# Kernel tuning notes

Hardware: AMD Instinct MI355X
Metric: run time of the kernel (lower is better)

## Reference

```python
import jax, jax.numpy as jnp
import numpy as np

MARGIN = 0.3
NUM_CLASSES = 1000


def setup_inputs() -> dict:
    key = jax.random.key(0)
    k1, k2 = jax.random.split(key)
    B, D = 8192, 256
    inputs = jax.random.normal(k1, (B, D), dtype=jnp.float32)
    targets = jax.random.randint(k2, (B,), 0, NUM_CLASSES, dtype=jnp.int64)
    return {"inputs": inputs, "targets": targets}


def reference(inputs, targets):
    # Squared Euclidean pairwise distances: ||x_i||^2 + ||x_j||^2 - 2 x_i.x_j
    sq = jnp.sum(inputs * inputs, axis=1)                      # [B]
    dist = sq[:, None] + sq[None, :] - 2.0 * (inputs @ inputs.T)  # [B, B]

    # Hard mining: per-row max over positives (same label, incl. self),
    # min over negatives, exactly as the torch per-row masked max/min loop.
    pos_mask = targets[:, None] == targets[None, :]            # [B, B] bool
    neg_inf = jnp.float32(-jnp.inf)
    pos_inf = jnp.float32(jnp.inf)
    dist_ap = jnp.max(jnp.where(pos_mask, dist, neg_inf), axis=1)  # [B]
    dist_an = jnp.min(jnp.where(pos_mask, pos_inf, dist), axis=1)  # [B]

    # MarginRankingLoss(margin)(dist_an, dist_ap, y=1) = mean relu(ap - an + m)
    loss = jnp.mean(jax.nn.relu(dist_ap - dist_an + MARGIN))
    prec = jnp.mean((dist_an > dist_ap).astype(jnp.float32))
    return (loss, prec)
```

## Files before the change

### kernel.cpp

```cpp
#include <hip/hip_runtime.h>
#include <hip/hip_bf16.h>

#define B_N 8192
#define D_K 256
#define MARGIN 0.3f

typedef float f32x4 __attribute__((ext_vector_type(4)));
typedef short s16x8 __attribute__((ext_vector_type(8)));

__device__ __forceinline__ unsigned fkey(float f) {
    unsigned u = __float_as_uint(f);
    return (u & 0x80000000u) ? ~u : (u | 0x80000000u);
}
__device__ __forceinline__ float kval(unsigned k) {
    return (k & 0x80000000u) ? __uint_as_float(k ^ 0x80000000u)
                             : __uint_as_float(~k);
}

__device__ __forceinline__ void load_lds16(const unsigned short* g,
                                           unsigned short* l) {
    __builtin_amdgcn_global_load_lds(
        (const __attribute__((address_space(1))) unsigned int*)g,
        (__attribute__((address_space(3))) unsigned int*)l, 16, 0, 0);
}

__global__ __launch_bounds__(256) void prep_kernel(const float* __restrict__ X,
        float* __restrict__ sq, unsigned* __restrict__ apk,
        unsigned* __restrict__ ank, unsigned short* __restrict__ Xp,
        float* __restrict__ acc2) {
    int row  = (blockIdx.x << 2) + (threadIdx.x >> 6);
    int lane = threadIdx.x & 63;
    const float4 v = reinterpret_cast<const float4*>(X + (size_t)row * D_K)[lane];

    float xs[4] = {v.x, v.y, v.z, v.w};
    ushort4 hv;
    unsigned short* hp = &hv.x;
    float s = 0.f;
    #pragma unroll
    for (int i = 0; i < 4; ++i) {
        __hip_bfloat16 h = __float2bfloat16(xs[i]);
        hp[i] = *reinterpret_cast<unsigned short*>(&h);
        float hf = __bfloat162float(h);
        s = fmaf(hf, hf, s);
    }
    *reinterpret_cast<ushort4*>(Xp + (size_t)row * D_K + lane * 4) = hv;

    #pragma unroll
    for (int o = 32; o > 0; o >>= 1) s += __shfl_down(s, o, 64);
    if (lane == 0) {
        sq[row]  = s;
        apk[row] = 0u;
        ank[row] = 0xFFFFFFFFu;
    }
    if (blockIdx.x == 0 && threadIdx.x == 0) {
        acc2[0] = 0.f; acc2[1] = 0.f;
        reinterpret_cast<unsigned*>(acc2)[2] = 0u;
    }
}

#define BM 128
#define BN 128

__global__ __launch_bounds__(256, 4) void dist_kernel(
        const unsigned short* __restrict__ Xp,
        const int* __restrict__ tgt, const float* __restrict__ sq,
        unsigned* __restrict__ apk, unsigned* __restrict__ ank) {
    __shared__ unsigned short Atile[128 * 64];
    __shared__ unsigned short Btile[128 * 64];

    const int t    = threadIdx.x;
    const int lane = t & 63;
    const int wave = t >> 6;
    const int wrow = (wave >> 1) * 64;
    const int wcol = (wave & 1) * 64;
    const int fr   = lane & 15;
    const int quad = lane >> 4;
    const float INF = __int_as_float(0x7f800000);

    int tt = blockIdx.x;
    int bx = (int)((sqrtf(8.f * (float)tt + 1.f) - 1.f) * 0.5f);
    while ((bx + 1) * (bx + 2) / 2 <= tt) ++bx;
    while (bx * (bx + 1) / 2 > tt) --bx;
    int by = tt - bx * (bx + 1) / 2;
    const int bm = by * BM;
    const int bn = bx * BN;

    const unsigned short* ag[4];
    const unsigned short* bg[4];
    unsigned short* al[4];
    unsigned short* bl[4];
    #pragma unroll
    for (int j = 0; j < 4; ++j) {
        int g = wave * 64 + j * 256 + lane;
        int r = g >> 3, s0 = g & 7;
        int u = s0 ^ (r & 7);
        ag[j] = Xp + (size_t)(bm + r) * D_K + u * 8;
        bg[j] = Xp + (size_t)(bn + r) * D_K + u * 8;
        al[j] = Atile + g * 8;
        bl[j] = Btile + g * 8;
    }

    f32x4 acc[4][4];
    #pragma unroll
    for (int i = 0; i < 4; ++i)
        #pragma unroll
        for (int j = 0; j < 4; ++j) acc[i][j] = (f32x4){0.f, 0.f, 0.f, 0.f};

    #pragma unroll 1
    for (int win = 0; win < 4; ++win) {
        __syncthreads();
        const int wo = win * 64;
        #pragma unroll
        for (int j = 0; j < 4; ++j) {
            load_lds16(ag[j] + wo, al[j]);
            load_lds16(bg[j] + wo, bl[j]);
        }
        __syncthreads();

        s16x8 a[4][2], b[4][2];
        #pragma unroll
        for (int mi = 0; mi < 4; ++mi) {
            int rb = (wrow + mi * 16 + fr) * 64;
            #pragma unroll
            for (int h = 0; h < 2; ++h) {
                int s = (h * 4 + quad) ^ (fr & 7);
                a[mi][h] = *reinterpret_cast<const s16x8*>(&Atile[rb + s * 8]);
            }
        }
        #pragma unroll
        for (int ni = 0; ni < 4; ++ni) {
            int rb = (wcol + ni * 16 + fr) * 64;
            #pragma unroll
            for (int h = 0; h < 2; ++h) {
                int s = (h * 4 + quad) ^ (fr & 7);
                b[ni][h] = *reinterpret_cast<const s16x8*>(&Btile[rb + s * 8]);
            }
        }
        #pragma unroll
        for (int mi = 0; mi < 4; ++mi)
            #pragma unroll
            for (int ni = 0; ni < 4; ++ni) {
                acc[mi][ni] = __builtin_amdgcn_mfma_f32_16x16x32_bf16(
                    a[mi][0], b[ni][0], acc[mi][ni], 0, 0, 0);
                acc[mi][ni] = __builtin_amdgcn_mfma_f32_16x16x32_bf16(
                    a[mi][1], b[ni][1], acc[mi][ni], 0, 0, 0);
            }
    }

    int   ct[4]; float csq[4];
    #pragma unroll
    for (int ni = 0; ni < 4; ++ni) {
        int c = bn + wcol + ni * 16 + fr;
        ct[ni] = tgt[c]; csq[ni] = sq[c];
    }
    float cap[4], can[4];
    #pragma unroll
    for (int ni = 0; ni < 4; ++ni) { cap[ni] = -INF; can[ni] = INF; }

    #pragma unroll
    for (int mi = 0; mi < 4; ++mi) {
        #pragma unroll
        for (int reg = 0; reg < 4; ++reg) {
            int rl = wrow + mi * 16 + quad * 4 + reg;
            int rt = tgt[bm + rl]; float rsq = sq[bm + rl];
            float rap = -INF, ran = INF;
            #pragma unroll
            for (int ni = 0; ni < 4; ++ni) {
                float d = rsq + csq[ni] - 2.f * acc[mi][ni][reg];
                bool pos = (rt == ct[ni]);
                if (pos) { rap = fmaxf(rap, d); cap[ni] = fmaxf(cap[ni], d); }
                else     { ran = fminf(ran, d); can[ni] = fminf(can[ni], d); }
            }
            #pragma unroll
            for (int o = 1; o < 16; o <<= 1) {
                rap = fmaxf(rap, __shfl_xor(rap, o, 64));
                ran = fminf(ran, __shfl_xor(ran, o, 64));
            }
            if (fr == 0) {
                atomicMax(&apk[bm + rl], fkey(rap));
                atomicMin(&ank[bm + rl], fkey(ran));
            }
        }
    }
    #pragma unroll
    for (int ni = 0; ni < 4; ++ni) {
        #pragma unroll
        for (int o = 16; o < 64; o <<= 1) {
            cap[ni] = fmaxf(cap[ni], __shfl_xor(cap[ni], o, 64));
            can[ni] = fminf(can[ni], __shfl_xor(can[ni], o, 64));
        }
    }
    if (lane < 16) {
        #pragma unroll
        for (int ni = 0; ni < 4; ++ni) {
            int c = bn + wcol + ni * 16 + lane;
            atomicMax(&apk[c], fkey(cap[ni]));
            atomicMin(&ank[c], fkey(can[ni]));
        }
    }
}

__global__ __launch_bounds__(256) void final_kernel(const unsigned* __restrict__ apk,
        const unsigned* __restrict__ ank, float* __restrict__ acc2,
        float* __restrict__ out) {
    __shared__ float s_sum[4], s_cnt[4];
    int i = blockIdx.x * 256 + threadIdx.x;
    float ap = kval(apk[i]);
    float an = kval(ank[i]);
    float v  = ap - an + MARGIN;
    float sum = v > 0.f ? v : 0.f;
    float cnt = an > ap ? 1.f : 0.f;
    #pragma unroll
    for (int o = 32; o > 0; o >>= 1) {
        sum += __shfl_down(sum, o, 64);
        cnt += __shfl_down(cnt, o, 64);
    }
    int wave = threadIdx.x >> 6, lane = threadIdx.x & 63;
    if (lane == 0) { s_sum[wave] = sum; s_cnt[wave] = cnt; }
    __syncthreads();
    if (threadIdx.x == 0) {
        float ts = 0.f, tc = 0.f;
        #pragma unroll
        for (int w = 0; w < 4; ++w) { ts += s_sum[w]; tc += s_cnt[w]; }
        atomicAdd(&acc2[0], ts);
        atomicAdd(&acc2[1], tc);
        __threadfence();
        unsigned ticket = atomicAdd(reinterpret_cast<unsigned*>(acc2) + 2, 1u);
        if (ticket == gridDim.x - 1) {
            float fs = atomicAdd(&acc2[0], 0.f);
            float fc = atomicAdd(&acc2[1], 0.f);
            out[0] = fs / (float)B_N;
            out[1] = fc / (float)B_N;
        }
    }
}

extern "C" void kernel_launch(void* const* d_in, const int* in_sizes, int n_in,
                              void* d_out, int out_size, void* d_ws, size_t ws_size,
                              hipStream_t stream) {
    const float* X   = (const float*)d_in[0];
    const int*   tgt = (const int*)d_in[1];

    char* ws = (char*)d_ws;
    float*          sq   = (float*)ws;
    unsigned*       apk  = (unsigned*)(ws + 32768);
    unsigned*       ank  = (unsigned*)(ws + 65536);
    float*          acc2 = (float*)(ws + 98304);
    unsigned short* Xp   = (unsigned short*)(ws + 131072);

    float* out = (float*)d_out;

    prep_kernel<<<B_N / 4, 256, 0, stream>>>(X, sq, apk, ank, Xp, acc2);
    dist_kernel<<<(64 * 65) / 2, 256, 0, stream>>>(Xp, tgt, sq, apk, ank);
    final_kernel<<<B_N / 256, 256, 0, stream>>>(apk, ank, acc2, out);
}
```

Measured before the change: 117.0 us.

## Fuse final reduction into dist kernel and reduce row partials via LDS

Removes the separate final kernel launch by having the last-finishing dist block, chosen by an atomic ticket, compute the loss and precision over all rows. Per-row max/min partials are no longer reduced with 16-lane shuffles plus per-wave atomics. They are staged in LDS (reusing the tile buffers) and reduced by one thread per row, so each block issues one atomic per row. This saves a launch and many global atomics, but adds extra barriers and a serial tail in the last block.

Result: slower. 142.3 us (+21.6%).

```diff
diff --git a/kernel.cpp b/kernel.cpp
--- a/kernel.cpp
+++ b/kernel.cpp
@@ -4,6 +4,7 @@
 #define B_N 8192
 #define D_K 256
 #define MARGIN 0.3f
+#define NBLK 2080
 
 typedef float f32x4 __attribute__((ext_vector_type(4)));
 typedef short s16x8 __attribute__((ext_vector_type(8)));
@@ -27,7 +28,7 @@
 __global__ __launch_bounds__(256) void prep_kernel(const float* __restrict__ X,
         float* __restrict__ sq, unsigned* __restrict__ apk,
         unsigned* __restrict__ ank, unsigned short* __restrict__ Xp,
-        float* __restrict__ acc2) {
+        unsigned* __restrict__ ticket) {
     int row  = (blockIdx.x << 2) + (threadIdx.x >> 6);
     int lane = threadIdx.x & 63;
     const float4 v = reinterpret_cast<const float4*>(X + (size_t)row * D_K)[lane];
@@ -52,10 +53,7 @@
         apk[row] = 0u;
         ank[row] = 0xFFFFFFFFu;
     }
-    if (blockIdx.x == 0 && threadIdx.x == 0) {
-        acc2[0] = 0.f; acc2[1] = 0.f;
-        reinterpret_cast<unsigned*>(acc2)[2] = 0u;
-    }
+    if (blockIdx.x == 0 && threadIdx.x == 0) *ticket = 0u;
 }
 
 #define BM 128
@@ -64,9 +62,12 @@
 __global__ __launch_bounds__(256, 4) void dist_kernel(
         const unsigned short* __restrict__ Xp,
         const int* __restrict__ tgt, const float* __restrict__ sq,
-        unsigned* __restrict__ apk, unsigned* __restrict__ ank) {
+        unsigned* __restrict__ apk, unsigned* __restrict__ ank,
+        unsigned* __restrict__ ticket, float* __restrict__ out) {
     __shared__ unsigned short Atile[128 * 64];
     __shared__ unsigned short Btile[128 * 64];
+    __shared__ float s_fin[8];
+    __shared__ unsigned s_go;
 
     const int t    = threadIdx.x;
     const int lane = t & 63;
@@ -157,6 +158,7 @@
     #pragma unroll
     for (int ni = 0; ni < 4; ++ni) { cap[ni] = -INF; can[ni] = INF; }
 
+    float rowap[4][4], rowan[4][4];
     #pragma unroll
     for (int mi = 0; mi < 4; ++mi) {
         #pragma unroll
@@ -171,17 +173,10 @@
                 if (pos) { rap = fmaxf(rap, d); cap[ni] = fmaxf(cap[ni], d); }
                 else     { ran = fminf(ran, d); can[ni] = fminf(can[ni], d); }
             }
-            #pragma unroll
-            for (int o = 1; o < 16; o <<= 1) {
-                rap = fmaxf(rap, __shfl_xor(rap, o, 64));
-                ran = fminf(ran, __shfl_xor(ran, o, 64));
-            }
-            if (fr == 0) {
-                atomicMax(&apk[bm + rl], fkey(rap));
-                atomicMin(&ank[bm + rl], fkey(ran));
-            }
-        }
-    }
+            rowap[mi][reg] = rap; rowan[mi][reg] = ran;
+        }
+    }
+
     #pragma unroll
     for (int ni = 0; ni < 4; ++ni) {
         #pragma unroll
@@ -198,39 +193,78 @@
             atomicMin(&ank[c], fkey(can[ni]));
         }
     }
-}
-
-__global__ __launch_bounds__(256) void final_kernel(const unsigned* __restrict__ apk,
-        const unsigned* __restrict__ ank, float* __restrict__ acc2,
-        float* __restrict__ out) {
-    __shared__ float s_sum[4], s_cnt[4];
-    int i = blockIdx.x * 256 + threadIdx.x;
-    float ap = kval(apk[i]);
-    float an = kval(ank[i]);
-    float v  = ap - an + MARGIN;
-    float sum = v > 0.f ? v : 0.f;
-    float cnt = an > ap ? 1.f : 0.f;
-    #pragma unroll
-    for (int o = 32; o > 0; o >>= 1) {
-        sum += __shfl_down(sum, o, 64);
-        cnt += __shfl_down(cnt, o, 64);
-    }
-    int wave = threadIdx.x >> 6, lane = threadIdx.x & 63;
-    if (lane == 0) { s_sum[wave] = sum; s_cnt[wave] = cnt; }
+
     __syncthreads();
-    if (threadIdx.x == 0) {
-        float ts = 0.f, tc = 0.f;
-        #pragma unroll
-        for (int w = 0; w < 4; ++w) { ts += s_sum[w]; tc += s_cnt[w]; }
-        atomicAdd(&acc2[0], ts);
-        atomicAdd(&acc2[1], tc);
+    float* sAP = reinterpret_cast<float*>(Atile);
+    float* sAN = reinterpret_cast<float*>(Btile);
+    {
+        const int w = wave & 1;
+        #pragma unroll
+        for (int mi = 0; mi < 4; ++mi)
+            #pragma unroll
+            for (int reg = 0; reg < 4; ++reg) {
+                int rl   = wrow + mi * 16 + quad * 4 + reg;
+                int slot = fr + 16 * ((w ^ quad) & 1);
+                sAP[rl * 32 + slot] = rowap[mi][reg];
+                sAN[rl * 32 + slot] = rowan[mi][reg];
+            }
+    }
+    __syncthreads();
+    {
+        int row = t & 127;
+        const float* src = (t < 128) ? sAP : sAN;
+        bool isMax = (t < 128);
+        f32x4 v0 = *reinterpret_cast<const f32x4*>(&src[row * 32 + ((t & 7) * 4)]);
+        #pragma unroll
+        for (int j = 1; j < 8; ++j) {
+            int c = ((t + j) & 7) * 4;
+            f32x4 v = *reinterpret_cast<const f32x4*>(&src[row * 32 + c]);
+            if (isMax) { v0.x = fmaxf(v0.x, v.x); v0.y = fmaxf(v0.y, v.y);
+                         v0.z = fmaxf(v0.z, v.z); v0.w = fmaxf(v0.w, v.w); }
+            else       { v0.x = fminf(v0.x, v.x); v0.y = fminf(v0.y, v.y);
+                         v0.z = fminf(v0.z, v.z); v0.w = fminf(v0.w, v.w); }
+        }
+        if (isMax) {
+            float m = fmaxf(fmaxf(v0.x, v0.y), fmaxf(v0.z, v0.w));
+            atomicMax(&apk[bm + row], fkey(m));
+        } else {
+            float m = fminf(fminf(v0.x, v0.y), fminf(v0.z, v0.w));
+            atomicMin(&ank[bm + row], fkey(m));
+        }
+    }
+
+    if (t == 0) {
         __threadfence();
-        unsigned ticket = atomicAdd(reinterpret_cast<unsigned*>(acc2) + 2, 1u);
-        if (ticket == gridDim.x - 1) {
-            float fs = atomicAdd(&acc2[0], 0.f);
-            float fc = atomicAdd(&acc2[1], 0.f);
-            out[0] = fs / (float)B_N;
-            out[1] = fc / (float)B_N;
+        unsigned tk = atomicAdd(ticket, 1u);
+        s_go = (tk == (unsigned)(gridDim.x - 1)) ? 1u : 0u;
+    }
+    __syncthreads();
+    if (s_go) {
+        __threadfence();
+        float sum = 0.f, cnt = 0.f;
+        for (int i = t; i < B_N; i += 256) {
+            unsigned ak = __hip_atomic_load(&apk[i], __ATOMIC_RELAXED,
+                                            __HIP_MEMORY_SCOPE_AGENT);
+            unsigned nk = __hip_atomic_load(&ank[i], __ATOMIC_RELAXED,
+                                            __HIP_MEMORY_SCOPE_AGENT);
+            float ap = kval(ak), an = kval(nk);
+            float v = ap - an + MARGIN;
+            if (v > 0.f) sum += v;
+            if (an > ap) cnt += 1.f;
+        }
+        #pragma unroll
+        for (int o = 32; o > 0; o >>= 1) {
+            sum += __shfl_down(sum, o, 64);
+            cnt += __shfl_down(cnt, o, 64);
+        }
+        if (lane == 0) { s_fin[wave] = sum; s_fin[4 + wave] = cnt; }
+        __syncthreads();
+        if (t == 0) {
+            float ts = 0.f, tc = 0.f;
+            #pragma unroll
+            for (int w = 0; w < 4; ++w) { ts += s_fin[w]; tc += s_fin[4 + w]; }
+            out[0] = ts / (float)B_N;
+            out[1] = tc / (float)B_N;
         }
     }
 }
@@ -242,15 +276,14 @@
     const int*   tgt = (const int*)d_in[1];
 
     char* ws = (char*)d_ws;
-    float*          sq   = (float*)ws;
-    unsigned*       apk  = (unsigned*)(ws + 32768);
-    unsigned*       ank  = (unsigned*)(ws + 65536);
-    float*          acc2 = (float*)(ws + 98304);
-    unsigned short* Xp   = (unsigned short*)(ws + 131072);
+    float*          sq     = (float*)ws;
+    unsigned*       apk    = (unsigned*)(ws + 32768);
+    unsigned*       ank    = (unsigned*)(ws + 65536);
+    unsigned*       ticket = (unsigned*)(ws + 98304);
+    unsigned short* Xp     = (unsigned short*)(ws + 131072);
 
     float* out = (float*)d_out;
 
-    prep_kernel<<<B_N / 4, 256, 0, stream>>>(X, sq, apk, ank, Xp, acc2);
-    dist_kernel<<<(64 * 65) / 2, 256, 0, stream>>>(Xp, tgt, sq, apk, ank);
-    final_kernel<<<B_N / 256, 256, 0, stream>>>(apk, ank, acc2, out);
-}
+    prep_kernel<<<B_N / 4, 256, 0, stream>>>(X, sq, apk, ank, Xp, ticket);
+    dist_kernel<<<NBLK, 256, 0, stream>>>(Xp, tgt, sq, apk, ank, ticket, out);
+}
```

## Double-buffer LDS tiles in the distance GEMM with K-step 32

Applied to the files above, without the earlier changes.

Replaces the single 64-wide K window, which needed two barriers per step, with two 32-wide LDS buffers. The loads for the next K slice are issued before computing on the current one, so each step needs one barrier and global-to-LDS traffic overlaps the MFMA work. The XOR swizzle on the LDS layout is dropped. The new 64-byte row stride may cause LDS bank conflicts on fragment reads, and the number of K iterations doubles.

Result: slower. 122.3 us (+4.5%).

```diff
diff --git a/kernel.cpp b/kernel.cpp
--- a/kernel.cpp
+++ b/kernel.cpp
@@ -4,6 +4,7 @@
 #define B_N 8192
 #define D_K 256
 #define MARGIN 0.3f
+#define NBLK 2080
 
 typedef float f32x4 __attribute__((ext_vector_type(4)));
 typedef short s16x8 __attribute__((ext_vector_type(8)));
@@ -65,8 +66,8 @@
         const unsigned short* __restrict__ Xp,
         const int* __restrict__ tgt, const float* __restrict__ sq,
         unsigned* __restrict__ apk, unsigned* __restrict__ ank) {
-    __shared__ unsigned short Atile[128 * 64];
-    __shared__ unsigned short Btile[128 * 64];
+    __shared__ unsigned short Ab[2][128 * 32];
+    __shared__ unsigned short Bb[2][128 * 32];
 
     const int t    = threadIdx.x;
     const int lane = t & 63;
@@ -85,19 +86,16 @@
     const int bm = by * BM;
     const int bn = bx * BN;
 
-    const unsigned short* ag[4];
-    const unsigned short* bg[4];
-    unsigned short* al[4];
-    unsigned short* bl[4];
-    #pragma unroll
-    for (int j = 0; j < 4; ++j) {
+    const unsigned short* ag[2];
+    const unsigned short* bg[2];
+    int ldso[2];
+    #pragma unroll
+    for (int j = 0; j < 2; ++j) {
         int g = wave * 64 + j * 256 + lane;
-        int r = g >> 3, s0 = g & 7;
-        int u = s0 ^ (r & 7);
+        int r = g >> 2, u = g & 3;
         ag[j] = Xp + (size_t)(bm + r) * D_K + u * 8;
         bg[j] = Xp + (size_t)(bn + r) * D_K + u * 8;
-        al[j] = Atile + g * 8;
-        bl[j] = Btile + g * 8;
+        ldso[j] = g * 8;
     }
 
     f32x4 acc[4][4];
@@ -106,45 +104,41 @@
         #pragma unroll
         for (int j = 0; j < 4; ++j) acc[i][j] = (f32x4){0.f, 0.f, 0.f, 0.f};
 
+    #pragma unroll
+    for (int j = 0; j < 2; ++j) {
+        load_lds16(ag[j], &Ab[0][ldso[j]]);
+        load_lds16(bg[j], &Bb[0][ldso[j]]);
+    }
+
     #pragma unroll 1
-    for (int win = 0; win < 4; ++win) {
+    for (int w = 0; w < 8; ++w) {
         __syncthreads();
-        const int wo = win * 64;
-        #pragma unroll
-        for (int j = 0; j < 4; ++j) {
-            load_lds16(ag[j] + wo, al[j]);
-            load_lds16(bg[j] + wo, bl[j]);
-        }
-        __syncthreads();
-
-        s16x8 a[4][2], b[4][2];
-        #pragma unroll
-        for (int mi = 0; mi < 4; ++mi) {
-            int rb = (wrow + mi * 16 + fr) * 64;
-            #pragma unroll
-            for (int h = 0; h < 2; ++h) {
-                int s = (h * 4 + quad) ^ (fr & 7);
-                a[mi][h] = *reinterpret_cast<const s16x8*>(&Atile[rb + s * 8]);
-            }
-        }
-        #pragma unroll
-        for (int ni = 0; ni < 4; ++ni) {
-            int rb = (wcol + ni * 16 + fr) * 64;
-            #pragma unroll
-            for (int h = 0; h < 2; ++h) {
-                int s = (h * 4 + quad) ^ (fr & 7);
-                b[ni][h] = *reinterpret_cast<const s16x8*>(&Btile[rb + s * 8]);
-            }
-        }
+        if (w < 7) {
+            const int ko = (w + 1) * 32;
+            #pragma unroll
+            for (int j = 0; j < 2; ++j) {
+                load_lds16(ag[j] + ko, &Ab[(w + 1) & 1][ldso[j]]);
+                load_lds16(bg[j] + ko, &Bb[(w + 1) & 1][ldso[j]]);
+            }
+        }
+        const unsigned short* At = Ab[w & 1];
+        const unsigned short* Bt = Bb[w & 1];
+
+        s16x8 a[4], b[4];
         #pragma unroll
         for (int mi = 0; mi < 4; ++mi)
-            #pragma unroll
-            for (int ni = 0; ni < 4; ++ni) {
+            a[mi] = *reinterpret_cast<const s16x8*>(
+                &At[(wrow + mi * 16 + fr) * 32 + quad * 8]);
+        #pragma unroll
+        for (int ni = 0; ni < 4; ++ni)
+            b[ni] = *reinterpret_cast<const s16x8*>(
+                &Bt[(wcol + ni * 16 + fr) * 32 + quad * 8]);
+        #pragma unroll
+        for (int mi = 0; mi < 4; ++mi)
+            #pragma unroll
+            for (int ni = 0; ni < 4; ++ni)
                 acc[mi][ni] = __builtin_amdgcn_mfma_f32_16x16x32_bf16(
-                    a[mi][0], b[ni][0], acc[mi][ni], 0, 0, 0);
-                acc[mi][ni] = __builtin_amdgcn_mfma_f32_16x16x32_bf16(
-                    a[mi][1], b[ni][1], acc[mi][ni], 0, 0, 0);
-            }
+                    a[mi], b[ni], acc[mi][ni], 0, 0, 0);
     }
 
     int   ct[4]; float csq[4];
@@ -251,6 +245,6 @@
     float* out = (float*)d_out;
 
     prep_kernel<<<B_N / 4, 256, 0, stream>>>(X, sq, apk, ank, Xp, acc2);
-    dist_kernel<<<(64 * 65) / 2, 256, 0, stream>>>(Xp, tgt, sq, apk, ank);
+    dist_kernel<<<NBLK, 256, 0, stream>>>(Xp, tgt, sq, apk, ank);
     final_kernel<<<B_N / 256, 256, 0, stream>>>(apk, ank, acc2, out);
 }
```
